# Performance work log

Hardware: AMD Instinct MI355X
Metric: run time of the kernel (lower is better)

## Reference

```python
import jax, jax.numpy as jnp
import numpy as np

N_NODES = 100000
N_EDGES = 1600000
N_GRAPHS = 512
IN_DIM = 128
HID = 128


def setup_inputs() -> dict:
    key = jax.random.key(0)
    ks = jax.random.split(key, 8)
    x = jax.random.normal(ks[0], (N_NODES, IN_DIM), dtype=jnp.float32)
    edge_index = jax.random.randint(ks[1], (2, N_EDGES), 0, N_NODES, dtype=jnp.int64)
    batch = jnp.sort(jax.random.randint(ks[2], (N_NODES,), 0, N_GRAPHS, dtype=jnp.int64))
    s1 = 1.0 / np.sqrt(IN_DIM)
    s2 = 1.0 / np.sqrt(HID)
    W1 = jax.random.normal(ks[3], (IN_DIM, HID), dtype=jnp.float32) * s1
    b1 = jnp.zeros((HID,), dtype=jnp.float32)
    W2 = jax.random.normal(ks[4], (HID, HID), dtype=jnp.float32) * s2
    b2 = jnp.zeros((HID,), dtype=jnp.float32)
    Wp = jax.random.normal(ks[5], (HID, 1), dtype=jnp.float32) * s2
    bp = jnp.zeros((1,), dtype=jnp.float32)
    return {"x": x, "edge_index": edge_index, "batch": batch,
            "W1": W1, "b1": b1, "W2": W2, "b2": b2, "Wp": Wp, "bp": bp}


def _gcn_conv(x, W, b, src, dst, deg_inv_sqrt):
    # PyG GCNConv: linear transform, then normalized scatter-add (self-loops
    # already appended to src/dst), then bias.
    h = x @ W                                   # [N, H]
    norm = deg_inv_sqrt[src] * deg_inv_sqrt[dst]  # [E+N]
    msg = h[src] * norm[:, None]                # gather + scale
    out = jax.ops.segment_sum(msg, dst, num_segments=N_NODES)
    return out + b


def reference(x, edge_index, batch, W1, b1, W2, b2, Wp, bp):
    # Add self-loops once; degree (with self-loops) over target nodes.
    si = jnp.arange(N_NODES, dtype=edge_index.dtype)
    src = jnp.concatenate([edge_index[0], si])
    dst = jnp.concatenate([edge_index[1], si])
    ones = jnp.ones(src.shape[0], dtype=x.dtype)
    deg = jax.ops.segment_sum(ones, dst, num_segments=N_NODES)
    deg_inv_sqrt = jnp.where(deg > 0, jax.lax.rsqrt(jnp.maximum(deg, 1.0)), 0.0)

    h = jax.nn.relu(_gcn_conv(x, W1, b1, src, dst, deg_inv_sqrt))  # dropout = identity (eval)
    h = jax.nn.relu(_gcn_conv(h, W2, b2, src, dst, deg_inv_sqrt))

    # global_mean_pool over graph ids
    sums = jax.ops.segment_sum(h, batch, num_segments=N_GRAPHS)
    cnts = jax.ops.segment_sum(jnp.ones(N_NODES, dtype=h.dtype), batch, num_segments=N_GRAPHS)
    pooled = sums / jnp.maximum(cnts, 1.0)[:, None]               # [G, H]

    return (pooled @ Wp + bp).squeeze(-1)                          # [G]
```

## Files before the change

### kernel.cpp

```cpp
#include <hip/hip_runtime.h>
#include <hip/hip_bf16.h>

#define NN 100000
#define NG 512
#define H  128

typedef _Float16 half8 __attribute__((ext_vector_type(8)));
typedef float f32x4 __attribute__((ext_vector_type(4)));

__global__ __launch_bounds__(256) void k_hist(const int* __restrict__ dst,
                                              int* __restrict__ deg, int E) {
    int e = blockIdx.x * 256 + threadIdx.x;
    if (e < E) atomicAdd(&deg[dst[e]], 1);
}

__global__ __launch_bounds__(256) void k_scan_block(const int* __restrict__ deg,
                                                    int* __restrict__ rowptr,
                                                    int* __restrict__ bsum, int n) {
    __shared__ int s[256];
    int tid = threadIdx.x;
    int i = blockIdx.x * 256 + tid;
    int v = (i < n) ? deg[i] : 0;
    s[tid] = v;
    __syncthreads();
    #pragma unroll
    for (int off = 1; off < 256; off <<= 1) {
        int t = (tid >= off) ? s[tid - off] : 0;
        __syncthreads();
        s[tid] += t;
        __syncthreads();
    }
    if (i < n) rowptr[i] = s[tid] - v;
    if (tid == 255) bsum[blockIdx.x] = s[255];
}

__global__ __launch_bounds__(512) void k_scan_top(int* __restrict__ bsum, int nb) {
    __shared__ int s[512];
    int tid = threadIdx.x;
    int v = (tid < nb) ? bsum[tid] : 0;
    s[tid] = v;
    __syncthreads();
    #pragma unroll
    for (int off = 1; off < 512; off <<= 1) {
        int t = (tid >= off) ? s[tid - off] : 0;
        __syncthreads();
        s[tid] += t;
        __syncthreads();
    }
    if (tid < nb) bsum[tid] = s[tid] - v;
}

__global__ __launch_bounds__(256) void k_scan_fin(int* __restrict__ rowptr,
                                                  const int* __restrict__ bsum,
                                                  const int* __restrict__ deg,
                                                  int* __restrict__ cursor,
                                                  float* __restrict__ dinv,
                                                  int n, int E) {
    int i = blockIdx.x * 256 + threadIdx.x;
    if (i >= n) return;
    int r = rowptr[i] + bsum[i >> 8];
    rowptr[i] = r;
    cursor[i] = r;
    dinv[i] = rsqrtf((float)deg[i] + 1.0f);
    if (i == 0) rowptr[n] = E;
}

__global__ __launch_bounds__(256) void k_wprep(const float* __restrict__ W1,
                                               const float* __restrict__ W2,
                                               _Float16* __restrict__ Wt1,
                                               _Float16* __restrict__ Wt2) {
    int bb = blockIdx.x;
    const float* W = (bb < 64) ? W1 : W2;
    _Float16* Wt = (bb < 64) ? Wt1 : Wt2;
    int i = (bb & 63) * 256 + threadIdx.x;
    int k = i >> 7, n = i & 127;
    Wt[n * 128 + k] = (_Float16)W[i];
}

__global__ __launch_bounds__(256) void k_fill_gemm1(
        const int* __restrict__ src, const int* __restrict__ dst,
        int* __restrict__ cursor, int* __restrict__ col, int E, int nfb,
        const float* __restrict__ x, const _Float16* __restrict__ Wt1,
        const float* __restrict__ dinv, _Float16* __restrict__ tS, int n) {
    if ((int)blockIdx.x < nfb) {
        int e = blockIdx.x * 256 + threadIdx.x;
        if (e >= E) return;
        int d = dst[e];
        int pos = atomicAdd(&cursor[d], 1);
        col[pos] = src[e];
        return;
    }
    const int row0 = ((int)blockIdx.x - nfb) * 64;
    const int tid = threadIdx.x;
    const int w = tid >> 6, lane = tid & 63;
    const int l16 = lane & 15, quad = lane >> 4;
    const int Arow = row0 + w * 16 + l16;
    f32x4 acc[8] = {};
    #pragma unroll
    for (int kk = 0; kk < 4; ++kk) {
        half8 af;
        if (Arow < n) {
            const float* ap = x + (size_t)Arow * H + kk * 32 + quad * 8;
            float4 a0 = ((const float4*)ap)[0];
            float4 a1 = ((const float4*)ap)[1];
            af[0] = (_Float16)a0.x; af[1] = (_Float16)a0.y;
            af[2] = (_Float16)a0.z; af[3] = (_Float16)a0.w;
            af[4] = (_Float16)a1.x; af[5] = (_Float16)a1.y;
            af[6] = (_Float16)a1.z; af[7] = (_Float16)a1.w;
        } else {
            #pragma unroll
            for (int j = 0; j < 8; ++j) af[j] = (_Float16)0.0f;
        }
        #pragma unroll
        for (int nt = 0; nt < 8; ++nt) {
            half8 bf = *((const half8*)(Wt1 + (nt * 16 + l16) * H + kk * 32 + quad * 8));
            acc[nt] = __builtin_amdgcn_mfma_f32_16x16x32_f16(af, bf, acc[nt], 0, 0, 0);
        }
    }
    #pragma unroll
    for (int r = 0; r < 4; ++r) {
        int R = row0 + w * 16 + quad * 4 + r;
        if (R < n) {
            float sc = dinv[R];
            _Float16* crow = tS + (size_t)R * H + l16;
            #pragma unroll
            for (int nt = 0; nt < 8; ++nt)
                crow[nt * 16] = (_Float16)(acc[nt][r] * sc);
        }
    }
}

__device__ __forceinline__ int bitonic64(int v, int lane) {
    #pragma unroll
    for (int k = 2; k <= 64; k <<= 1) {
        #pragma unroll
        for (int j = k >> 1; j > 0; j >>= 1) {
            int p = __shfl_xor(v, j);
            bool up = ((lane & k) == 0);
            bool keepmin = (((lane & j) == 0) == up);
            v = keepmin ? min(v, p) : max(v, p);
        }
    }
    return v;
}

__device__ __forceinline__ void gather_rows_h(const half8* __restrict__ t8,
                                              const int* __restrict__ col,
                                              int node, int e0, int end,
                                              float acc[8]) {
    const int lane = threadIdx.x & 63;
    const int q = lane >> 4;
    const int l16 = lane & 15;
    float a0[8] = {}, a1[8] = {};
    if (q == 0) {
        half8 v = t8[(size_t)node * 16 + l16];
        #pragma unroll
        for (int i = 0; i < 8; ++i) a0[i] = (float)v[i];
    }
    const bool small = (end - e0) <= 64;
    for (int base = e0; base < end; base += 64) {
        int ce = base + lane;
        int cidx = (ce < end) ? col[ce] : 0x7fffffff;
        if (small) cidx = bitonic64(cidx, lane);
        int m = min(64, end - base);
        int nf = m >> 2;
        int g = 0;
        for (; g + 2 <= nf; g += 2) {
            int s0 = __shfl(cidx, 4 * g + q);
            int s1 = __shfl(cidx, 4 * g + 4 + q);
            half8 v0 = t8[(size_t)s0 * 16 + l16];
            half8 v1 = t8[(size_t)s1 * 16 + l16];
            #pragma unroll
            for (int i = 0; i < 8; ++i) {
                a0[i] += (float)v0[i];
                a1[i] += (float)v1[i];
            }
        }
        if (g < nf) {
            int s0 = __shfl(cidx, 4 * g + q);
            half8 v0 = t8[(size_t)s0 * 16 + l16];
            #pragma unroll
            for (int i = 0; i < 8; ++i) a0[i] += (float)v0[i];
        }
        int tail = m & 3;
        if (tail) {
            int s = __shfl(cidx, 4 * nf + q);
            if (q < tail) {
                half8 v = t8[(size_t)s * 16 + l16];
                #pragma unroll
                for (int i = 0; i < 8; ++i) a0[i] += (float)v[i];
            }
        }
    }
    #pragma unroll
    for (int i = 0; i < 8; ++i) {
        float t = a0[i] + a1[i];
        t += __shfl_xor(t, 16);
        t += __shfl_xor(t, 32);
        acc[i] = t;
    }
}

#define LDA 136
__global__ __launch_bounds__(256) void k_gather1f(const _Float16* __restrict__ tS,
                                                  const int* __restrict__ rowptr,
                                                  const int* __restrict__ col,
                                                  const float* __restrict__ dinv,
                                                  const float* __restrict__ b,
                                                  const _Float16* __restrict__ Wt2,
                                                  _Float16* __restrict__ tS2, int n) {
    __shared__ _Float16 As[64 * LDA];
    const int tid = threadIdx.x;
    const int w = tid >> 6, lane = tid & 63;
    const int q = lane >> 4, l16 = lane & 15, quad = lane >> 4;
    const int node0 = blockIdx.x * 64;
    const float4* b4 = (const float4*)b;
    float4 bb0 = b4[2 * l16], bb1 = b4[2 * l16 + 1];

    for (int i = 0; i < 16; ++i) {
        int node = node0 + w * 16 + i;
        half8 hv;
        #pragma unroll
        for (int j = 0; j < 8; ++j) hv[j] = (_Float16)0.0f;
        if (node < n) {
            int e0 = rowptr[node], end = rowptr[node + 1];
            float acc[8];
            gather_rows_h((const half8*)tS, col, node, e0, end, acc);
            float dn = dinv[node];
            hv[0] = (_Float16)fmaxf(dn * acc[0] + bb0.x, 0.0f);
            hv[1] = (_Float16)fmaxf(dn * acc[1] + bb0.y, 0.0f);
            hv[2] = (_Float16)fmaxf(dn * acc[2] + bb0.z, 0.0f);
            hv[3] = (_Float16)fmaxf(dn * acc[3] + bb0.w, 0.0f);
            hv[4] = (_Float16)fmaxf(dn * acc[4] + bb1.x, 0.0f);
            hv[5] = (_Float16)fmaxf(dn * acc[5] + bb1.y, 0.0f);
            hv[6] = (_Float16)fmaxf(dn * acc[6] + bb1.z, 0.0f);
            hv[7] = (_Float16)fmaxf(dn * acc[7] + bb1.w, 0.0f);
        }
        if (q == 0)
            *((half8*)(As + (w * 16 + i) * LDA + l16 * 8)) = hv;
    }
    __syncthreads();

    f32x4 acc2[8] = {};
    const _Float16* aBase = As + (w * 16 + l16) * LDA + quad * 8;
    #pragma unroll
    for (int kk = 0; kk < 4; ++kk) {
        half8 af = *((const half8*)(aBase + kk * 32));
        #pragma unroll
        for (int nt = 0; nt < 8; ++nt) {
            half8 bf = *((const half8*)(Wt2 + (nt * 16 + l16) * H + kk * 32 + quad * 8));
            acc2[nt] = __builtin_amdgcn_mfma_f32_16x16x32_f16(af, bf, acc2[nt], 0, 0, 0);
        }
    }
    #pragma unroll
    for (int r = 0; r < 4; ++r) {
        int R = node0 + w * 16 + quad * 4 + r;
        if (R < n) {
            float sc = dinv[R];
            _Float16* crow = tS2 + (size_t)R * H + l16;
            #pragma unroll
            for (int nt = 0; nt < 8; ++nt)
                crow[nt * 16] = (_Float16)(acc2[nt][r] * sc);
        }
    }
}

__global__ __launch_bounds__(256) void k_gather2(const _Float16* __restrict__ tS,
                                                 const int* __restrict__ rowptr,
                                                 const int* __restrict__ col,
                                                 const float* __restrict__ dinv,
                                                 const float* __restrict__ b,
                                                 const float* __restrict__ Wp,
                                                 const int* __restrict__ batch,
                                                 float* __restrict__ pool,
                                                 float* __restrict__ cnt, int n) {
    int node = blockIdx.x * 4 + (threadIdx.x >> 6);
    int lane = threadIdx.x & 63;
    int l16 = lane & 15;
    if (node >= n) return;
    int e0 = rowptr[node], end = rowptr[node + 1];
    float acc[8];
    gather_rows_h((const half8*)tS, col, node, e0, end, acc);
    float dn = dinv[node];
    const float4* b4 = (const float4*)b;
    const float4* w4 = (const float4*)Wp;
    float4 bb0 = b4[2 * l16], bb1 = b4[2 * l16 + 1];
    float4 wp0 = w4[2 * l16], wp1 = w4[2 * l16 + 1];
    float s = fmaxf(dn * acc[0] + bb0.x, 0.0f) * wp0.x +
              fmaxf(dn * acc[1] + bb0.y, 0.0f) * wp0.y +
              fmaxf(dn * acc[2] + bb0.z, 0.0f) * wp0.z +
              fmaxf(dn * acc[3] + bb0.w, 0.0f) * wp0.w +
              fmaxf(dn * acc[4] + bb1.x, 0.0f) * wp1.x +
              fmaxf(dn * acc[5] + bb1.y, 0.0f) * wp1.y +
              fmaxf(dn * acc[6] + bb1.z, 0.0f) * wp1.z +
              fmaxf(dn * acc[7] + bb1.w, 0.0f) * wp1.w;
    s += __shfl_xor(s, 1);
    s += __shfl_xor(s, 2);
    s += __shfl_xor(s, 4);
    s += __shfl_xor(s, 8);
    if (lane == 0) {
        int g = batch[node];
        atomicAdd(&pool[g], s);
        atomicAdd(&cnt[g], 1.0f);
    }
}

__global__ __launch_bounds__(256) void final_out_kernel(const float* __restrict__ pool,
                                                        const float* __restrict__ cnt,
                                                        const float* __restrict__ bp,
                                                        float* __restrict__ out, int g) {
    int i = blockIdx.x * 256 + threadIdx.x;
    if (i < g) out[i] = pool[i] / fmaxf(cnt[i], 1.0f) + bp[0];
}

extern "C" void kernel_launch(void* const* d_in, const int* in_sizes, int n_in,
                              void* d_out, int out_size, void* d_ws, size_t ws_size,
                              hipStream_t stream) {
    const float* x     = (const float*)d_in[0];
    const int*   ei    = (const int*)d_in[1];
    const int*   batch = (const int*)d_in[2];
    const float* W1    = (const float*)d_in[3];
    const float* b1    = (const float*)d_in[4];
    const float* W2    = (const float*)d_in[5];
    const float* b2    = (const float*)d_in[6];
    const float* Wp    = (const float*)d_in[7];
    const float* bp    = (const float*)d_in[8];
    float* out = (float*)d_out;

    const int E = in_sizes[1] / 2;
    const int* src = ei;
    const int* dst = ei + E;

    const size_t BUFH = (size_t)NN * H * sizeof(_Float16);
    const size_t NI   = 401408;
    char* ws = (char*)d_ws;
    size_t off = 0;
    _Float16* tS   = (_Float16*)(ws + off); off += BUFH;
    _Float16* tS2  = (_Float16*)(ws + off); off += BUFH;
    int*      deg  = (int*)     (ws + off); off += NI;
    int*   rowptr  = (int*)     (ws + off); off += NI;
    int*   cursor  = (int*)     (ws + off); off += NI;
    float*    dinv = (float*)   (ws + off); off += NI;
    int*      col  = (int*)     (ws + off); off += ((size_t)E * 4 + 4095) / 4096 * 4096;
    _Float16* Wt1  = (_Float16*)(ws + off); off += 32768;
    _Float16* Wt2  = (_Float16*)(ws + off); off += 32768;
    int*      bsum = (int*)     (ws + off); off += 4096;
    float*    pool = (float*)   (ws + off); off += 2048;
    float*    cnt  = (float*)   (ws + off); off += 2048;

    const int NB  = (NN + 255) / 256;
    const int NFB = (E + 255) / 256;
    const int NGB = (NN + 63) / 64;

    hipMemsetAsync(deg, 0, NN * sizeof(int), stream);
    hipMemsetAsync(pool, 0, 4096, stream);
    k_wprep<<<128, 256, 0, stream>>>(W1, W2, Wt1, Wt2);
    k_hist<<<NFB, 256, 0, stream>>>(dst, deg, E);
    k_scan_block<<<NB, 256, 0, stream>>>(deg, rowptr, bsum, NN);
    k_scan_top<<<1, 512, 0, stream>>>(bsum, NB);
    k_scan_fin<<<NB, 256, 0, stream>>>(rowptr, bsum, deg, cursor, dinv, NN, E);

    k_fill_gemm1<<<NFB + NGB, 256, 0, stream>>>(src, dst, cursor, col, E, NFB,
                                                x, Wt1, dinv, tS, NN);

    k_gather1f<<<NGB, 256, 0, stream>>>(tS, rowptr, col, dinv, b1, Wt2, tS2, NN);

    k_gather2<<<(NN + 3) / 4, 256, 0, stream>>>(tS2, rowptr, col, dinv, b2, Wp,
                                                batch, pool, cnt, NN);

    final_out_kernel<<<(NG + 255) / 256, 256, 0, stream>>>(pool, cnt, bp, out, NG);
}
```

Measured before the change: 732.4 us.

## Split fused gather+GEMM2 into per-node gather and separate GEMM kernel; drop bitonic sort

Replaces the fused layer-1 gather plus layer-2 GEMM kernel (one block per 64 nodes, each wave looping over 16 nodes serially) with a per-node gather kernel that writes h1 to a new global buffer, followed by a standalone MFMA GEMM kernel. It also removes the bitonic sort of neighbor indices before gathering. The aim is more parallelism and latency hiding in the gather phase. The cost is an extra 25.6MB write and read of h1 and one more kernel launch, and gathers become less sorted, which may hurt cache locality.

```diff
diff --git a/kernel.cpp b/kernel.cpp
--- a/kernel.cpp
+++ b/kernel.cpp
@@ -130,18 +130,42 @@
     }
 }
 
-__device__ __forceinline__ int bitonic64(int v, int lane) {
-    #pragma unroll
-    for (int k = 2; k <= 64; k <<= 1) {
+__global__ __launch_bounds__(256) void k_gemm2(const _Float16* __restrict__ h1,
+                                               const _Float16* __restrict__ Wt2,
+                                               const float* __restrict__ dinv,
+                                               _Float16* __restrict__ tS2, int n) {
+    const int row0 = blockIdx.x * 64;
+    const int tid = threadIdx.x;
+    const int w = tid >> 6, lane = tid & 63;
+    const int l16 = lane & 15, quad = lane >> 4;
+    const int Arow = row0 + w * 16 + l16;
+    f32x4 acc[8] = {};
+    #pragma unroll
+    for (int kk = 0; kk < 4; ++kk) {
+        half8 af;
+        if (Arow < n) {
+            af = ((const half8*)(h1 + (size_t)Arow * H))[kk * 4 + quad];
+        } else {
+            #pragma unroll
+            for (int j = 0; j < 8; ++j) af[j] = (_Float16)0.0f;
+        }
         #pragma unroll
-        for (int j = k >> 1; j > 0; j >>= 1) {
-            int p = __shfl_xor(v, j);
-            bool up = ((lane & k) == 0);
-            bool keepmin = (((lane & j) == 0) == up);
-            v = keepmin ? min(v, p) : max(v, p);
-        }
-    }
-    return v;
+        for (int nt = 0; nt < 8; ++nt) {
+            half8 bf = *((const half8*)(Wt2 + (nt * 16 + l16) * H + kk * 32 + quad * 8));
+            acc[nt] = __builtin_amdgcn_mfma_f32_16x16x32_f16(af, bf, acc[nt], 0, 0, 0);
+        }
+    }
+    #pragma unroll
+    for (int r = 0; r < 4; ++r) {
+        int R = row0 + w * 16 + quad * 4 + r;
+        if (R < n) {
+            float sc = dinv[R];
+            _Float16* crow = tS2 + (size_t)R * H + l16;
+            #pragma unroll
+            for (int nt = 0; nt < 8; ++nt)
+                crow[nt * 16] = (_Float16)(acc[nt][r] * sc);
+        }
+    }
 }
 
 __device__ __forceinline__ void gather_rows_h(const half8* __restrict__ t8,
@@ -157,11 +181,9 @@
         #pragma unroll
         for (int i = 0; i < 8; ++i) a0[i] = (float)v[i];
     }
-    const bool small = (end - e0) <= 64;
     for (int base = e0; base < end; base += 64) {
         int ce = base + lane;
-        int cidx = (ce < end) ? col[ce] : 0x7fffffff;
-        if (small) cidx = bitonic64(cidx, lane);
+        int cidx = (ce < end) ? col[ce] : 0;
         int m = min(64, end - base);
         int nf = m >> 2;
         int g = 0;
@@ -201,67 +223,33 @@
     }
 }
 
-#define LDA 136
-__global__ __launch_bounds__(256) void k_gather1f(const _Float16* __restrict__ tS,
-                                                  const int* __restrict__ rowptr,
-                                                  const int* __restrict__ col,
-                                                  const float* __restrict__ dinv,
-                                                  const float* __restrict__ b,
-                                                  const _Float16* __restrict__ Wt2,
-                                                  _Float16* __restrict__ tS2, int n) {
-    __shared__ _Float16 As[64 * LDA];
-    const int tid = threadIdx.x;
-    const int w = tid >> 6, lane = tid & 63;
-    const int q = lane >> 4, l16 = lane & 15, quad = lane >> 4;
-    const int node0 = blockIdx.x * 64;
-    const float4* b4 = (const float4*)b;
-    float4 bb0 = b4[2 * l16], bb1 = b4[2 * l16 + 1];
-
-    for (int i = 0; i < 16; ++i) {
-        int node = node0 + w * 16 + i;
+__global__ __launch_bounds__(256) void k_gather1(const _Float16* __restrict__ tS,
+                                                 const int* __restrict__ rowptr,
+                                                 const int* __restrict__ col,
+                                                 const float* __restrict__ dinv,
+                                                 const float* __restrict__ b,
+                                                 _Float16* __restrict__ out, int n) {
+    int node = blockIdx.x * 4 + (threadIdx.x >> 6);
+    int lane = threadIdx.x & 63;
+    int q = lane >> 4, l16 = lane & 15;
+    if (node >= n) return;
+    int e0 = rowptr[node], end = rowptr[node + 1];
+    float acc[8];
+    gather_rows_h((const half8*)tS, col, node, e0, end, acc);
+    if (q == 0) {
+        float dn = dinv[node];
+        const float4* b4 = (const float4*)b;
+        float4 bb0 = b4[2 * l16], bb1 = b4[2 * l16 + 1];
         half8 hv;
-        #pragma unroll
-        for (int j = 0; j < 8; ++j) hv[j] = (_Float16)0.0f;
-        if (node < n) {
-            int e0 = rowptr[node], end = rowptr[node + 1];
-            float acc[8];
-            gather_rows_h((const half8*)tS, col, node, e0, end, acc);
-            float dn = dinv[node];
-            hv[0] = (_Float16)fmaxf(dn * acc[0] + bb0.x, 0.0f);
-            hv[1] = (_Float16)fmaxf(dn * acc[1] + bb0.y, 0.0f);
-            hv[2] = (_Float16)fmaxf(dn * acc[2] + bb0.z, 0.0f);
-            hv[3] = (_Float16)fmaxf(dn * acc[3] + bb0.w, 0.0f);
-            hv[4] = (_Float16)fmaxf(dn * acc[4] + bb1.x, 0.0f);
-            hv[5] = (_Float16)fmaxf(dn * acc[5] + bb1.y, 0.0f);
-            hv[6] = (_Float16)fmaxf(dn * acc[6] + bb1.z, 0.0f);
-            hv[7] = (_Float16)fmaxf(dn * acc[7] + bb1.w, 0.0f);
-        }
-        if (q == 0)
-            *((half8*)(As + (w * 16 + i) * LDA + l16 * 8)) = hv;
-    }
-    __syncthreads();
-
-    f32x4 acc2[8] = {};
-    const _Float16* aBase = As + (w * 16 + l16) * LDA + quad * 8;
-    #pragma unroll
-    for (int kk = 0; kk < 4; ++kk) {
-        half8 af = *((const half8*)(aBase + kk * 32));
-        #pragma unroll
-        for (int nt = 0; nt < 8; ++nt) {
-            half8 bf = *((const half8*)(Wt2 + (nt * 16 + l16) * H + kk * 32 + quad * 8));
-            acc2[nt] = __builtin_amdgcn_mfma_f32_16x16x32_f16(af, bf, acc2[nt], 0, 0, 0);
-        }
-    }
-    #pragma unroll
-    for (int r = 0; r < 4; ++r) {
-        int R = node0 + w * 16 + quad * 4 + r;
-        if (R < n) {
-            float sc = dinv[R];
-            _Float16* crow = tS2 + (size_t)R * H + l16;
-            #pragma unroll
-            for (int nt = 0; nt < 8; ++nt)
-                crow[nt * 16] = (_Float16)(acc2[nt][r] * sc);
-        }
+        hv[0] = (_Float16)fmaxf(dn * acc[0] + bb0.x, 0.0f);
+        hv[1] = (_Float16)fmaxf(dn * acc[1] + bb0.y, 0.0f);
+        hv[2] = (_Float16)fmaxf(dn * acc[2] + bb0.z, 0.0f);
+        hv[3] = (_Float16)fmaxf(dn * acc[3] + bb0.w, 0.0f);
+        hv[4] = (_Float16)fmaxf(dn * acc[4] + bb1.x, 0.0f);
+        hv[5] = (_Float16)fmaxf(dn * acc[5] + bb1.y, 0.0f);
+        hv[6] = (_Float16)fmaxf(dn * acc[6] + bb1.z, 0.0f);
+        hv[7] = (_Float16)fmaxf(dn * acc[7] + bb1.w, 0.0f);
+        ((half8*)out)[(size_t)node * 16 + l16] = hv;
     }
 }
 
@@ -336,6 +324,7 @@
     char* ws = (char*)d_ws;
     size_t off = 0;
     _Float16* tS   = (_Float16*)(ws + off); off += BUFH;
+    _Float16* h1   = (_Float16*)(ws + off); off += BUFH;
     _Float16* tS2  = (_Float16*)(ws + off); off += BUFH;
     int*      deg  = (int*)     (ws + off); off += NI;
     int*   rowptr  = (int*)     (ws + off); off += NI;
@@ -363,7 +352,8 @@
     k_fill_gemm1<<<NFB + NGB, 256, 0, stream>>>(src, dst, cursor, col, E, NFB,
                                                 x, Wt1, dinv, tS, NN);
 
-    k_gather1f<<<NGB, 256, 0, stream>>>(tS, rowptr, col, dinv, b1, Wt2, tS2, NN);
+    k_gather1<<<(NN + 3) / 4, 256, 0, stream>>>(tS, rowptr, col, dinv, b1, h1, NN);
+    k_gemm2<<<NGB, 256, 0, stream>>>(h1, Wt2, dinv, tS2, NN);
 
     k_gather2<<<(NN + 3) / 4, 256, 0, stream>>>(tS2, rowptr, col, dinv, b2, Wp,
                                                 batch, pool, cnt, NN);
```

After: 688.0 us. 6.1% less time.
